# Kernel tuning notes

Measured on AMD Instinct MI355X. Metric: run time of the kernel, lower is better.

Reference implementation:

```python
import jax, jax.numpy as jnp
import numpy as np

EMBED_DIM = 128
B, SQ, SKV = 16, 2048, 2048


def setup_inputs() -> dict:
    key = jax.random.key(0)
    ks = jax.random.split(key, 8)
    d = EMBED_DIM
    scale = 1.0 / np.sqrt(d)
    return {
        "x": jax.random.normal(ks[0], (B, SQ, d), dtype=jnp.float32),
        "y": jax.random.normal(ks[1], (B, SKV, d), dtype=jnp.float32),
        "Wq": jax.random.normal(ks[2], (d, d), dtype=jnp.float32) * scale,
        "bq": jax.random.normal(ks[3], (d,), dtype=jnp.float32) * 0.02,
        "Wk": jax.random.normal(ks[4], (d, d), dtype=jnp.float32) * scale,
        "bk": jax.random.normal(ks[5], (d,), dtype=jnp.float32) * 0.02,
        "Wv": jax.random.normal(ks[6], (d, d), dtype=jnp.float32) * scale,
        "bv": jax.random.normal(ks[7], (d,), dtype=jnp.float32) * 0.02,
    }


def reference(x, y, Wq, bq, Wk, bk, Wv, bv):
    # Linear projections (torch Linear: x @ W.T + b; here W stored as [in,out])
    q = x @ Wq + bq            # [B, SQ, d]
    k = y @ Wk + bk            # [B, SKV, d]
    v = y @ Wv + bv            # [B, SKV, d]
    # Source scales by q.size(-1)**0.5 = sqrt(embed_dim)
    inv_scale = 1.0 / jnp.sqrt(jnp.asarray(q.shape[-1], q.dtype))
    scores = jnp.einsum("bqd,bkd->bqk", q, k) * inv_scale  # [B, SQ, SKV]
    attn = jax.nn.softmax(scores, axis=-1)
    return jnp.einsum("bqk,bkd->bqd", attn, v)
```

## Files before the change

kernel.cpp:

```cpp
#include <hip/hip_runtime.h>
#include <hip/hip_bf16.h>

typedef unsigned short ushort_t;
typedef __attribute__((ext_vector_type(8))) short short8;
typedef __attribute__((ext_vector_type(4))) float f32x4;
typedef __attribute__((ext_vector_type(16))) float f32x16;

#define MFMA16(a, b, c) __builtin_amdgcn_mfma_f32_16x16x32_bf16((a), (b), (c), 0, 0, 0)
#define MFMA32(a, b, c) __builtin_amdgcn_mfma_f32_32x32x16_bf16((a), (b), (c), 0, 0, 0)

__device__ __forceinline__ ushort_t f2bf(float f) {
    return __builtin_bit_cast(ushort_t, __float2bfloat16(f));
}

#define CVTPK(lo, hi) ({ unsigned int r_; \
    asm("v_cvt_pk_bf16_f32 %0, %1, %2" : "=v"(r_) : "v"(lo), "v"(hi)); r_; })

__device__ __forceinline__ void gl_lds16(const void* g, void* l) {
    __builtin_amdgcn_global_load_lds((const __attribute__((address_space(1))) void*)g,
                                     (__attribute__((address_space(3))) void*)l, 16, 0, 0);
}

__global__ __launch_bounds__(256) void wt_kernel(
    const float* __restrict__ Wq, const float* __restrict__ Wk, const float* __restrict__ Wv,
    ushort_t* __restrict__ WTq, ushort_t* __restrict__ WTk, ushort_t* __restrict__ WTv)
{
    __shared__ __align__(16) ushort_t wt2[128 * 24];

    const int mat  = blockIdx.x >> 3;
    const int slab = blockIdx.x & 7;
    const float* W = (mat == 0) ? Wq : (mat == 1) ? Wk : Wv;
    ushort_t*   WT = (mat == 0) ? WTq : (mat == 1) ? WTk : WTv;

    const int t = threadIdx.x;
    #pragma unroll
    for (int i = 0; i < 2; ++i) {
        int idx = t + i * 256;
        int kloc = idx >> 5;
        int c0   = (idx & 31) * 4;
        f32x4 v = ((const f32x4*)(W + (size_t)(slab * 16) * 128))[idx];
        #pragma unroll
        for (int j = 0; j < 4; ++j)
            wt2[(c0 + j) * 24 + kloc] = f2bf(v[j]);
    }
    __syncthreads();
    const int r    = t >> 1;
    const int half = t & 1;
    short8 v8 = *(const short8*)&wt2[r * 24 + half * 8];
    *(short8*)(WT + r * 128 + slab * 16 + half * 8) = v8;
}

__global__ __launch_bounds__(256) void proj_all(
    const float* __restrict__ x, const float* __restrict__ y,
    const ushort_t* __restrict__ WTq, const float* __restrict__ bq,
    const ushort_t* __restrict__ WTk, const float* __restrict__ bk,
    const ushort_t* __restrict__ WTv, const float* __restrict__ bv,
    ushort_t* __restrict__ Qd, ushort_t* __restrict__ Kd, ushort_t* __restrict__ VTd,
    float qscale)
{
    __shared__ __align__(16) char smem[34816];

    const int t = threadIdx.x;
    const bool isQ = blockIdx.x < 512;
    const int pb = isQ ? blockIdx.x : (blockIdx.x - 512);
    const float* src = isQ ? x : y;

    const int w  = t >> 6;
    const int l  = t & 63;
    const int lg = l >> 4;
    const int ln = l & 15;
    const int acol = lg * 8;

    {
        const char* srcb = (const char*)(src + (size_t)(pb * 64) * 128);
        #pragma unroll
        for (int i = 0; i < 8; ++i) {
            int off = i * 4096 + w * 1024 + l * 16;
            int soff = off ^ (((off >> 9) & 7) << 4);
            gl_lds16(srcb + soff, smem + i * 4096 + w * 1024);
        }
    }
    __syncthreads();

    short8 afrag[4];
    {
        const int row = w * 16 + ln;
        const int sw = (row & 7) << 4;
        #pragma unroll
        for (int kc = 0; kc < 4; ++kc) {
            int off0 = row * 512 + lg * 32 + kc * 128;
            f32x4 a0 = *(const f32x4*)(smem + (off0 ^ sw));
            f32x4 a1 = *(const f32x4*)(smem + ((off0 + 16) ^ sw));
            short8 a;
            #pragma unroll
            for (int j = 0; j < 4; ++j) { a[j] = (short)f2bf(a0[j]); a[4 + j] = (short)f2bf(a1[j]); }
            afrag[kc] = a;
        }
    }
    __syncthreads();

    ushort_t* tile = (ushort_t*)smem;
    ushort_t* vt   = (ushort_t*)(smem + 18432);

    const ushort_t* WT1 = isQ ? WTq : WTk;
    const float*    b1  = isQ ? bq  : bk;
    const float     sc  = isQ ? qscale : 1.0f;

    #pragma unroll
    for (int ct = 0; ct < 8; ++ct) {
        f32x4 acc = {0.f, 0.f, 0.f, 0.f};
        const int c = ct * 16 + ln;
        #pragma unroll
        for (int kc = 0; kc < 4; ++kc) {
            short8 bfr = *(const short8*)(WT1 + c * 128 + kc * 32 + acol);
            acc = MFMA16(afrag[kc], bfr, acc);
        }
        float bvv = b1[c];
        #pragma unroll
        for (int reg = 0; reg < 4; ++reg)
            tile[(w * 16 + lg * 4 + reg) * 144 + c] = f2bf((acc[reg] + bvv) * sc);
    }

    if (!isQ) {
        #pragma unroll
        for (int ct = 0; ct < 8; ++ct) {
            f32x4 acc = {0.f, 0.f, 0.f, 0.f};
            const int c = ct * 16 + ln;
            #pragma unroll
            for (int kc = 0; kc < 4; ++kc) {
                short8 bfr = *(const short8*)(WTv + c * 128 + kc * 32 + acol);
                acc = MFMA16(afrag[kc], bfr, acc);
            }
            float bvv = bv[c];
            #pragma unroll
            for (int reg = 0; reg < 4; ++reg) {
                int rloc = w * 16 + lg * 4 + reg;
                int byte = (c * 128 + rloc * 2) ^ ((c & 7) << 4);
                *(ushort_t*)((char*)vt + byte) = f2bf(acc[reg] + bvv);
            }
        }
    }
    __syncthreads();

    {
        const int row = t >> 2, ch = t & 3;
        ushort_t* dst1 = (isQ ? Qd : Kd) + (size_t)(pb * 64 + row) * 128 + ch * 32;
        #pragma unroll
        for (int j = 0; j < 4; ++j)
            *(short8*)(dst1 + j * 8) = *(const short8*)&tile[row * 144 + ch * 32 + j * 8];
    }
    if (!isQ) {
        const int r0b = pb * 64;
        const int b   = r0b >> 11;
        const int kv0 = r0b & 2047;
        const int c    = t >> 1;
        const int half = t & 1;
        ushort_t* dst = VTd + (size_t)b * 128 * 2048 + (size_t)c * 2048 + kv0 + half * 32;
        #pragma unroll
        for (int j = 0; j < 4; ++j) {
            int byte = (c * 128 + (half * 32 + j * 8) * 2) ^ ((c & 7) << 4);
            *(short8*)(dst + j * 8) = *(const short8*)((const char*)vt + byte);
        }
    }
}

#define KVBLK 64
#define NT (2048 / KVBLK)
__global__ __launch_bounds__(256) void attn_kernel(
    const ushort_t* __restrict__ Q, const ushort_t* __restrict__ K,
    const ushort_t* __restrict__ VT, float* __restrict__ out)
{
    __shared__ __align__(16) char smem_[65536];

    const int t = threadIdx.x;
    const int bid = (int)blockIdx.x;
    const int wg = (bid & 7) * 64 + (bid >> 3);
    const int b  = wg >> 5;
    const int q0blk = (wg & 31) * 64;

    const char* Kb  = (const char*)(K  + (size_t)b * 2048 * 128);
    const char* VTb = (const char*)(VT + (size_t)b * 128 * 2048);
    const ushort_t* Qb = Q + (size_t)b * 2048 * 128;

    const int w   = t >> 6;
    const int qg  = w >> 1;
    const int kvh = w & 1;
    const int l  = t & 63;
    const int lq = l & 31;
    const int h  = l >> 5;
    const int q0 = q0blk + qg * 32;

    short8 qfrag[8];
    {
        const ushort_t* qp = Qb + (size_t)(q0 + lq) * 128 + h * 8;
        #pragma unroll
        for (int kc = 0; kc < 8; ++kc)
            qfrag[kc] = *(const short8*)(qp + kc * 16);
    }

    f32x16 o[4];
    #pragma unroll
    for (int db = 0; db < 4; ++db)
        #pragma unroll
        for (int i = 0; i < 16; ++i) o[db][i] = 0.f;
    f32x16 ls;
    #pragma unroll
    for (int i = 0; i < 16; ++i) ls[i] = 0.f;

    auto stage = [&](int buf, int kt) {
        const char* kb = Kb + (size_t)kt * KVBLK * 256;
        const int kv2 = kt * KVBLK * 2;
        char* kd = smem_ + buf * 16384;
        char* vd = smem_ + 32768 + buf * 16384;
        #pragma unroll
        for (int i = 0; i < 4; ++i) {
            int base = w * 4096 + i * 1024;
            int p = base + l * 16;
            int pl = p ^ (((p >> 8) & 15) << 4);
            gl_lds16(kb + pl, kd + base);
            int dv = ((pl >> 8) << 1) | ((pl >> 7) & 1);
            gl_lds16(VTb + (size_t)dv * 4096 + kv2 + (pl & 127), vd + base);
        }
    };

    stage(0, 0);
    int cur = 0;

    for (int kt = 0; kt < NT; ++kt) {
        __syncthreads();
        if (kt + 1 < NT) stage(cur ^ 1, kt + 1);

        const char* klp = smem_ + cur * 16384;
        f32x16 s;
        #pragma unroll
        for (int i = 0; i < 16; ++i) s[i] = 0.f;
        const int krow = kvh * 32 + lq;
        const int ksw = (krow & 15) << 4;
        __builtin_amdgcn_s_setprio(1);
        #pragma unroll
        for (int kc = 0; kc < 8; ++kc) {
            int col = (h * 16 + kc * 32) ^ ksw;
            short8 kf = *(const short8*)(klp + krow * 256 + col);
            s = MFMA32(kf, qfrag[kc], s);
        }
        __builtin_amdgcn_s_setprio(0);

        #pragma unroll
        for (int i = 0; i < 16; ++i) s[i] = __builtin_exp2f(s[i]);
        #pragma unroll
        for (int i = 0; i < 16; ++i) ls[i] += s[i];

        short8 pf[2];
        {
            auto pack = [&](int a, short8& outf) {
                unsigned u0 = CVTPK(s[a * 8 + 0], s[a * 8 + 1]);
                unsigned u1 = CVTPK(s[a * 8 + 2], s[a * 8 + 3]);
                unsigned u2 = CVTPK(s[a * 8 + 4], s[a * 8 + 5]);
                unsigned u3 = CVTPK(s[a * 8 + 6], s[a * 8 + 7]);
                unsigned x0 = __shfl_xor(u0, 32);
                unsigned x1 = __shfl_xor(u1, 32);
                unsigned x2 = __shfl_xor(u2, 32);
                unsigned x3 = __shfl_xor(u3, 32);
                union { unsigned wds[4]; short8 s8; } f;
                f.wds[0] = h ? x2 : u0;
                f.wds[1] = h ? x3 : u1;
                f.wds[2] = h ? u2 : x0;
                f.wds[3] = h ? u3 : x1;
                outf = f.s8;
            };
            pack(0, pf[0]);
            pack(1, pf[1]);
        }

        const char* vlp = smem_ + 32768 + cur * 16384;
        __builtin_amdgcn_s_setprio(1);
        #pragma unroll
        for (int db = 0; db < 4; ++db) {
            int d = db * 32 + lq;
            int vrow = d >> 1;
            int vsw = (vrow & 15) << 4;
            #pragma unroll
            for (int ks = 0; ks < 2; ++ks) {
                int colb = ((d & 1) << 7) | (kvh * 64 + ks * 32 + h * 16);
                short8 vf = *(const short8*)(vlp + vrow * 256 + (colb ^ vsw));
                o[db] = MFMA32(vf, pf[ks], o[db]);
            }
        }
        __builtin_amdgcn_s_setprio(0);
        cur ^= 1;
    }

    float lsum;
    {
        float a8[8];
        #pragma unroll
        for (int i = 0; i < 8; ++i) a8[i] = ls[i] + ls[i + 8];
        #pragma unroll
        for (int i = 0; i < 4; ++i) a8[i] += a8[i + 4];
        lsum = (a8[0] + a8[1]) + (a8[2] + a8[3]);
    }
    lsum += __shfl_xor(lsum, 32);

    __syncthreads();
    float* mrg = (float*)smem_;
    const int mo = qg * 4224 + lq * 132;
    const int mlb = 8448;

    if (kvh == 1) {
        #pragma unroll
        for (int db = 0; db < 4; ++db) {
            #pragma unroll
            for (int rq = 0; rq < 4; ++rq) {
                f32x4 v4;
                #pragma unroll
                for (int j = 0; j < 4; ++j) v4[j] = o[db][rq * 4 + j];
                *(f32x4*)&mrg[mo + db * 32 + rq * 8 + 4 * h] = v4;
            }
        }
        if (h == 0) mrg[mlb + qg * 64 + lq] = lsum;
    }
    __syncthreads();
    if (kvh == 0) {
        float inv = 1.0f / (lsum + mrg[mlb + qg * 64 + lq]);
        float* ob = out + (size_t)b * 2048 * 128 + (size_t)(q0 + lq) * 128;
        #pragma unroll
        for (int db = 0; db < 4; ++db) {
            #pragma unroll
            for (int rq = 0; rq < 4; ++rq) {
                f32x4 p4 = *(const f32x4*)&mrg[mo + db * 32 + rq * 8 + 4 * h];
                f32x4 st;
                #pragma unroll
                for (int j = 0; j < 4; ++j)
                    st[j] = (o[db][rq * 4 + j] + p4[j]) * inv;
                *(f32x4*)(ob + db * 32 + rq * 8 + 4 * h) = st;
            }
        }
    }
}

extern "C" void kernel_launch(void* const* d_in, const int* in_sizes, int n_in,
                              void* d_out, int out_size, void* d_ws, size_t ws_size,
                              hipStream_t stream) {
    (void)in_sizes; (void)n_in; (void)out_size; (void)ws_size;
    const float* x  = (const float*)d_in[0];
    const float* y  = (const float*)d_in[1];
    const float* Wq = (const float*)d_in[2];
    const float* bq = (const float*)d_in[3];
    const float* Wk = (const float*)d_in[4];
    const float* bk = (const float*)d_in[5];
    const float* Wv = (const float*)d_in[6];
    const float* bv = (const float*)d_in[7];
    float* out = (float*)d_out;

    ushort_t* wtq = (ushort_t*)d_out;
    ushort_t* wtk = wtq + 16384;
    ushort_t* wtv = wtk + 16384;

    ushort_t* qws  = (ushort_t*)d_ws;
    ushort_t* kws  = qws + (size_t)32768 * 128;
    ushort_t* vtws = kws + (size_t)32768 * 128;

    const float qscale = (float)(1.4426950408889634 / 11.313708498984761);

    wt_kernel<<<24, 256, 0, stream>>>(Wq, Wk, Wv, wtq, wtk, wtv);
    proj_all<<<1024, 256, 0, stream>>>(x, y, wtq, bq, wtk, bk, wtv, bv, qws, kws, vtws, qscale);
    attn_kernel<<<512, 256, 0, stream>>>(qws, kws, vtws, out);
}
```

Baseline: 99.89 us.

## Fuse Q projection into attention kernel and use permlane32 swap for P packing

The Q projection moves out of the projection kernel and into the attention prologue. Each attention block loads its 64 rows of x into LDS, projects them with MFMA, and reads its Q fragments from a swizzled LDS tile, so Q is never written to or read back from global memory. The projection kernel now handles only K and V, with half the blocks. The P fragment packing also replaces four shfl_xor calls and their selects with two v_permlane32_swap instructions, and the transposed weights move from the output buffer into the workspace. The cost is extra prologue work and barriers in each attention block before its main loop starts.

```diff
diff --git a/kernel.cpp b/kernel.cpp
--- a/kernel.cpp
+++ b/kernel.cpp
@@ -50,20 +50,16 @@
     *(short8*)(WT + r * 128 + slab * 16 + half * 8) = v8;
 }
 
-__global__ __launch_bounds__(256) void proj_all(
-    const float* __restrict__ x, const float* __restrict__ y,
-    const ushort_t* __restrict__ WTq, const float* __restrict__ bq,
+__global__ __launch_bounds__(256) void projKV(
+    const float* __restrict__ y,
     const ushort_t* __restrict__ WTk, const float* __restrict__ bk,
     const ushort_t* __restrict__ WTv, const float* __restrict__ bv,
-    ushort_t* __restrict__ Qd, ushort_t* __restrict__ Kd, ushort_t* __restrict__ VTd,
-    float qscale)
+    ushort_t* __restrict__ Kd, ushort_t* __restrict__ VTd)
 {
     __shared__ __align__(16) char smem[34816];
 
     const int t = threadIdx.x;
-    const bool isQ = blockIdx.x < 512;
-    const int pb = isQ ? blockIdx.x : (blockIdx.x - 512);
-    const float* src = isQ ? x : y;
+    const int pb = blockIdx.x;
 
     const int w  = t >> 6;
     const int l  = t & 63;
@@ -72,7 +68,7 @@
     const int acol = lg * 8;
 
     {
-        const char* srcb = (const char*)(src + (size_t)(pb * 64) * 128);
+        const char* srcb = (const char*)(y + (size_t)(pb * 64) * 128);
         #pragma unroll
         for (int i = 0; i < 8; ++i) {
             int off = i * 4096 + w * 1024 + l * 16;
@@ -102,54 +98,48 @@
     ushort_t* tile = (ushort_t*)smem;
     ushort_t* vt   = (ushort_t*)(smem + 18432);
 
-    const ushort_t* WT1 = isQ ? WTq : WTk;
-    const float*    b1  = isQ ? bq  : bk;
-    const float     sc  = isQ ? qscale : 1.0f;
-
     #pragma unroll
     for (int ct = 0; ct < 8; ++ct) {
         f32x4 acc = {0.f, 0.f, 0.f, 0.f};
         const int c = ct * 16 + ln;
         #pragma unroll
         for (int kc = 0; kc < 4; ++kc) {
-            short8 bfr = *(const short8*)(WT1 + c * 128 + kc * 32 + acol);
+            short8 bfr = *(const short8*)(WTk + c * 128 + kc * 32 + acol);
             acc = MFMA16(afrag[kc], bfr, acc);
         }
-        float bvv = b1[c];
+        float bvv = bk[c];
         #pragma unroll
         for (int reg = 0; reg < 4; ++reg)
-            tile[(w * 16 + lg * 4 + reg) * 144 + c] = f2bf((acc[reg] + bvv) * sc);
-    }
-
-    if (!isQ) {
-        #pragma unroll
-        for (int ct = 0; ct < 8; ++ct) {
-            f32x4 acc = {0.f, 0.f, 0.f, 0.f};
-            const int c = ct * 16 + ln;
-            #pragma unroll
-            for (int kc = 0; kc < 4; ++kc) {
-                short8 bfr = *(const short8*)(WTv + c * 128 + kc * 32 + acol);
-                acc = MFMA16(afrag[kc], bfr, acc);
-            }
-            float bvv = bv[c];
-            #pragma unroll
-            for (int reg = 0; reg < 4; ++reg) {
-                int rloc = w * 16 + lg * 4 + reg;
-                int byte = (c * 128 + rloc * 2) ^ ((c & 7) << 4);
-                *(ushort_t*)((char*)vt + byte) = f2bf(acc[reg] + bvv);
-            }
+            tile[(w * 16 + lg * 4 + reg) * 144 + c] = f2bf(acc[reg] + bvv);
+    }
+
+    #pragma unroll
+    for (int ct = 0; ct < 8; ++ct) {
+        f32x4 acc = {0.f, 0.f, 0.f, 0.f};
+        const int c = ct * 16 + ln;
+        #pragma unroll
+        for (int kc = 0; kc < 4; ++kc) {
+            short8 bfr = *(const short8*)(WTv + c * 128 + kc * 32 + acol);
+            acc = MFMA16(afrag[kc], bfr, acc);
+        }
+        float bvv = bv[c];
+        #pragma unroll
+        for (int reg = 0; reg < 4; ++reg) {
+            int rloc = w * 16 + lg * 4 + reg;
+            int byte = (c * 128 + rloc * 2) ^ ((c & 7) << 4);
+            *(ushort_t*)((char*)vt + byte) = f2bf(acc[reg] + bvv);
         }
     }
     __syncthreads();
 
     {
         const int row = t >> 2, ch = t & 3;
-        ushort_t* dst1 = (isQ ? Qd : Kd) + (size_t)(pb * 64 + row) * 128 + ch * 32;
+        ushort_t* dst1 = Kd + (size_t)(pb * 64 + row) * 128 + ch * 32;
         #pragma unroll
         for (int j = 0; j < 4; ++j)
             *(short8*)(dst1 + j * 8) = *(const short8*)&tile[row * 144 + ch * 32 + j * 8];
     }
-    if (!isQ) {
+    {
         const int r0b = pb * 64;
         const int b   = r0b >> 11;
         const int kv0 = r0b & 2047;
@@ -167,8 +157,10 @@
 #define KVBLK 64
 #define NT (2048 / KVBLK)
 __global__ __launch_bounds__(256) void attn_kernel(
-    const ushort_t* __restrict__ Q, const ushort_t* __restrict__ K,
-    const ushort_t* __restrict__ VT, float* __restrict__ out)
+    const float* __restrict__ X, const ushort_t* __restrict__ WTq,
+    const float* __restrict__ bq, float qscale,
+    const ushort_t* __restrict__ K, const ushort_t* __restrict__ VT,
+    float* __restrict__ out)
 {
     __shared__ __align__(16) char smem_[65536];
 
@@ -180,7 +172,6 @@
 
     const char* Kb  = (const char*)(K  + (size_t)b * 2048 * 128);
     const char* VTb = (const char*)(VT + (size_t)b * 128 * 2048);
-    const ushort_t* Qb = Q + (size_t)b * 2048 * 128;
 
     const int w   = t >> 6;
     const int qg  = w >> 1;
@@ -188,14 +179,63 @@
     const int l  = t & 63;
     const int lq = l & 31;
     const int h  = l >> 5;
-    const int q0 = q0blk + qg * 32;
 
     short8 qfrag[8];
     {
-        const ushort_t* qp = Qb + (size_t)(q0 + lq) * 128 + h * 8;
-        #pragma unroll
-        for (int kc = 0; kc < 8; ++kc)
-            qfrag[kc] = *(const short8*)(qp + kc * 16);
+        const char* srcb = (const char*)(X + (size_t)(b * 2048 + q0blk) * 128);
+        #pragma unroll
+        for (int i = 0; i < 8; ++i) {
+            int off = i * 4096 + w * 1024 + l * 16;
+            int soff = off ^ (((off >> 9) & 7) << 4);
+            gl_lds16(srcb + soff, smem_ + i * 4096 + w * 1024);
+        }
+        __syncthreads();
+
+        const int lg = l >> 4, ln = l & 15;
+        short8 afrag[4];
+        {
+            const int row = w * 16 + ln;
+            const int sw = (row & 7) << 4;
+            #pragma unroll
+            for (int kc = 0; kc < 4; ++kc) {
+                int off0 = row * 512 + lg * 32 + kc * 128;
+                f32x4 a0 = *(const f32x4*)(smem_ + (off0 ^ sw));
+                f32x4 a1 = *(const f32x4*)(smem_ + ((off0 + 16) ^ sw));
+                short8 a;
+                #pragma unroll
+                for (int j = 0; j < 4; ++j) { a[j] = (short)f2bf(a0[j]); a[4 + j] = (short)f2bf(a1[j]); }
+                afrag[kc] = a;
+            }
+        }
+        char* qtile = smem_ + 32768;
+        #pragma unroll
+        for (int ct = 0; ct < 8; ++ct) {
+            f32x4 acc = {0.f, 0.f, 0.f, 0.f};
+            const int c = ct * 16 + ln;
+            #pragma unroll
+            for (int kc = 0; kc < 4; ++kc) {
+                short8 bfr = *(const short8*)(WTq + c * 128 + kc * 32 + lg * 8);
+                acc = MFMA16(afrag[kc], bfr, acc);
+            }
+            float bvv = bq[c];
+            #pragma unroll
+            for (int reg = 0; reg < 4; ++reg) {
+                int row = w * 16 + lg * 4 + reg;
+                int byte = (row * 256 + c * 2) ^ ((row & 15) << 4);
+                *(ushort_t*)(qtile + byte) = f2bf((acc[reg] + bvv) * qscale);
+            }
+        }
+        __syncthreads();
+        {
+            const int row = qg * 32 + lq;
+            const int sw = (row & 15) << 4;
+            #pragma unroll
+            for (int kc = 0; kc < 8; ++kc) {
+                int byte = (row * 256 + kc * 32 + h * 16) ^ sw;
+                qfrag[kc] = *(const short8*)(qtile + byte);
+            }
+        }
+        __syncthreads();
     }
 
     f32x16 o[4];
@@ -252,24 +292,19 @@
 
         short8 pf[2];
         {
-            auto pack = [&](int a, short8& outf) {
+            auto pack2 = [&](int a, short8& outf) {
                 unsigned u0 = CVTPK(s[a * 8 + 0], s[a * 8 + 1]);
                 unsigned u1 = CVTPK(s[a * 8 + 2], s[a * 8 + 3]);
                 unsigned u2 = CVTPK(s[a * 8 + 4], s[a * 8 + 5]);
                 unsigned u3 = CVTPK(s[a * 8 + 6], s[a * 8 + 7]);
-                unsigned x0 = __shfl_xor(u0, 32);
-                unsigned x1 = __shfl_xor(u1, 32);
-                unsigned x2 = __shfl_xor(u2, 32);
-                unsigned x3 = __shfl_xor(u3, 32);
+                asm("v_permlane32_swap_b32 %0, %1" : "+v"(u0), "+v"(u2));
+                asm("v_permlane32_swap_b32 %0, %1" : "+v"(u1), "+v"(u3));
                 union { unsigned wds[4]; short8 s8; } f;
-                f.wds[0] = h ? x2 : u0;
-                f.wds[1] = h ? x3 : u1;
-                f.wds[2] = h ? u2 : x0;
-                f.wds[3] = h ? u3 : x1;
+                f.wds[0] = u0; f.wds[1] = u1; f.wds[2] = u2; f.wds[3] = u3;
                 outf = f.s8;
             };
-            pack(0, pf[0]);
-            pack(1, pf[1]);
+            pack2(0, pf[0]);
+            pack2(1, pf[1]);
         }
 
         const char* vlp = smem_ + 32768 + cur * 16384;
@@ -305,6 +340,7 @@
     float* mrg = (float*)smem_;
     const int mo = qg * 4224 + lq * 132;
     const int mlb = 8448;
+    const int q0 = q0blk + qg * 32;
 
     if (kvh == 1) {
         #pragma unroll
@@ -352,17 +388,15 @@
     const float* bv = (const float*)d_in[7];
     float* out = (float*)d_out;
 
-    ushort_t* wtq = (ushort_t*)d_out;
+    ushort_t* wtq = (ushort_t*)d_ws;
     ushort_t* wtk = wtq + 16384;
     ushort_t* wtv = wtk + 16384;
-
-    ushort_t* qws  = (ushort_t*)d_ws;
-    ushort_t* kws  = qws + (size_t)32768 * 128;
+    ushort_t* kws  = (ushort_t*)d_ws + 65536;
     ushort_t* vtws = kws + (size_t)32768 * 128;
 
     const float qscale = (float)(1.4426950408889634 / 11.313708498984761);
 
     wt_kernel<<<24, 256, 0, stream>>>(Wq, Wk, Wv, wtq, wtk, wtv);
-    proj_all<<<1024, 256, 0, stream>>>(x, y, wtq, bq, wtk, bk, wtv, bv, qws, kws, vtws, qscale);
-    attn_kernel<<<512, 256, 0, stream>>>(qws, kws, vtws, out);
-}
+    projKV<<<512, 256, 0, stream>>>(y, wtk, bk, wtv, bv, kws, vtws);
+    attn_kernel<<<512, 256, 0, stream>>>(x, wtq, bq, qscale, kws, vtws, out);
+}
```

Result: no change. 101.5 us (+1.6%).

## Use three rotating LDS buffers with split K/V staging and permlane32 swaps

Applied to the files above, without the earlier changes.

Replaces the double-buffered K+V staging (64KB LDS) with three rotating 16KB buffers. K and V loads for the next tile are issued separately, each after a barrier guarded by an explicit vmcnt wait, so prefetch overlaps the QK and PV phases more finely and LDS use drops, which could allow higher occupancy. It also replaces four shfl_xor plus selects with two v_permlane32_swap instructions when packing P fragments. The hand-placed vmcnt counts and buffer rotation are fragile, and the final iteration prefetches tile 0 only to discard it.

```diff
diff --git a/kernel.cpp b/kernel.cpp
--- a/kernel.cpp
+++ b/kernel.cpp
@@ -170,7 +170,7 @@
     const ushort_t* __restrict__ Q, const ushort_t* __restrict__ K,
     const ushort_t* __restrict__ VT, float* __restrict__ out)
 {
-    __shared__ __align__(16) char smem_[65536];
+    __shared__ __align__(16) char smem_[49152];
 
     const int t = threadIdx.x;
     const int bid = (int)blockIdx.x;
@@ -207,30 +207,42 @@
     #pragma unroll
     for (int i = 0; i < 16; ++i) ls[i] = 0.f;
 
-    auto stage = [&](int buf, int kt) {
+    auto stageK = [&](char* kd, int kt) {
         const char* kb = Kb + (size_t)kt * KVBLK * 256;
-        const int kv2 = kt * KVBLK * 2;
-        char* kd = smem_ + buf * 16384;
-        char* vd = smem_ + 32768 + buf * 16384;
         #pragma unroll
         for (int i = 0; i < 4; ++i) {
             int base = w * 4096 + i * 1024;
             int p = base + l * 16;
             int pl = p ^ (((p >> 8) & 15) << 4);
             gl_lds16(kb + pl, kd + base);
+        }
+    };
+    auto stageV = [&](char* vd, int kt) {
+        const int kv2 = kt * KVBLK * 2;
+        #pragma unroll
+        for (int i = 0; i < 4; ++i) {
+            int base = w * 4096 + i * 1024;
+            int p = base + l * 16;
+            int pl = p ^ (((p >> 8) & 15) << 4);
             int dv = ((pl >> 8) << 1) | ((pl >> 7) & 1);
             gl_lds16(VTb + (size_t)dv * 4096 + kv2 + (pl & 127), vd + base);
         }
     };
 
-    stage(0, 0);
-    int cur = 0;
+    char* bK = smem_;
+    char* bV = smem_ + 16384;
+    char* bN = smem_ + 32768;
+
+    stageK(bK, 0);
+    stageV(bV, 0);
 
     for (int kt = 0; kt < NT; ++kt) {
-        __syncthreads();
-        if (kt + 1 < NT) stage(cur ^ 1, kt + 1);
-
-        const char* klp = smem_ + cur * 16384;
+        const int ktn = (kt + 1 < NT) ? kt + 1 : 0;
+
+        asm volatile("s_waitcnt vmcnt(4)" ::: "memory");
+        __builtin_amdgcn_s_barrier();
+        stageK(bN, ktn);
+
         f32x16 s;
         #pragma unroll
         for (int i = 0; i < 16; ++i) s[i] = 0.f;
@@ -240,7 +252,7 @@
         #pragma unroll
         for (int kc = 0; kc < 8; ++kc) {
             int col = (h * 16 + kc * 32) ^ ksw;
-            short8 kf = *(const short8*)(klp + krow * 256 + col);
+            short8 kf = *(const short8*)(bK + krow * 256 + col);
             s = MFMA32(kf, qfrag[kc], s);
         }
         __builtin_amdgcn_s_setprio(0);
@@ -252,27 +264,25 @@
 
         short8 pf[2];
         {
-            auto pack = [&](int a, short8& outf) {
+            auto pack2 = [&](int a, short8& outf) {
                 unsigned u0 = CVTPK(s[a * 8 + 0], s[a * 8 + 1]);
                 unsigned u1 = CVTPK(s[a * 8 + 2], s[a * 8 + 3]);
                 unsigned u2 = CVTPK(s[a * 8 + 4], s[a * 8 + 5]);
                 unsigned u3 = CVTPK(s[a * 8 + 6], s[a * 8 + 7]);
-                unsigned x0 = __shfl_xor(u0, 32);
-                unsigned x1 = __shfl_xor(u1, 32);
-                unsigned x2 = __shfl_xor(u2, 32);
-                unsigned x3 = __shfl_xor(u3, 32);
+                asm("v_permlane32_swap_b32 %0, %1" : "+v"(u0), "+v"(u2));
+                asm("v_permlane32_swap_b32 %0, %1" : "+v"(u1), "+v"(u3));
                 union { unsigned wds[4]; short8 s8; } f;
-                f.wds[0] = h ? x2 : u0;
-                f.wds[1] = h ? x3 : u1;
-                f.wds[2] = h ? u2 : x0;
-                f.wds[3] = h ? u3 : x1;
+                f.wds[0] = u0; f.wds[1] = u1; f.wds[2] = u2; f.wds[3] = u3;
                 outf = f.s8;
             };
-            pack(0, pf[0]);
-            pack(1, pf[1]);
-        }
-
-        const char* vlp = smem_ + 32768 + cur * 16384;
+            pack2(0, pf[0]);
+            pack2(1, pf[1]);
+        }
+
+        asm volatile("s_waitcnt vmcnt(4)" ::: "memory");
+        __builtin_amdgcn_s_barrier();
+        stageV(bK, ktn);
+
         __builtin_amdgcn_s_setprio(1);
         #pragma unroll
         for (int db = 0; db < 4; ++db) {
@@ -282,13 +292,16 @@
             #pragma unroll
             for (int ks = 0; ks < 2; ++ks) {
                 int colb = ((d & 1) << 7) | (kvh * 64 + ks * 32 + h * 16);
-                short8 vf = *(const short8*)(vlp + vrow * 256 + (colb ^ vsw));
+                short8 vf = *(const short8*)(bV + vrow * 256 + (colb ^ vsw));
                 o[db] = MFMA32(vf, pf[ks], o[db]);
             }
         }
         __builtin_amdgcn_s_setprio(0);
-        cur ^= 1;
-    }
+
+        char* tmp = bK; bK = bN; bN = bV; bV = tmp;
+    }
+
+    asm volatile("s_waitcnt vmcnt(0)" ::: "memory");
 
     float lsum;
     {
```

Result: faster. 95.92 us (-4.0%).
